# Performance work log

Hardware: AMD Instinct MI355X
Metric: run time of the kernel (lower is better)

The kernel has to match this reference:

```python
import jax, jax.numpy as jnp
import numpy as np

NUM_GRAPHS = 64


def gcn_conv(x, edge_index, W, b):
    # PyG GCNConv: x' = D^-1/2 (A+I) D^-1/2 (x W) + b, self-loops added.
    n = x.shape[0]
    h = x @ W  # [N, out]
    loop = jnp.arange(n)
    src = jnp.concatenate([edge_index[0], loop])
    dst = jnp.concatenate([edge_index[1], loop])
    deg = jax.ops.segment_sum(jnp.ones_like(dst, dtype=h.dtype), dst, num_segments=n)
    dinv = jnp.where(deg > 0, jax.lax.rsqrt(deg), 0.0)
    norm = dinv[src] * dinv[dst]  # [E+N]
    msgs = h[src] * norm[:, None]  # gather + scale
    out = jax.ops.segment_sum(msgs, dst, num_segments=n)  # scatter-add
    return out + b


def lstm_step(x, W_ih, W_hh, b_ih, b_hh):
    # single time step, zero initial state; PyTorch gate order i,f,g,o
    H = W_hh.shape[1]
    gates = x @ W_ih.T + b_ih + b_hh  # h0 = 0 so W_hh term vanishes
    i, f, g, o = jnp.split(gates, 4, axis=-1)
    i, f, o = jax.nn.sigmoid(i), jax.nn.sigmoid(f), jax.nn.sigmoid(o)
    c = i * jnp.tanh(g)  # f * c0 = 0
    return o * jnp.tanh(c)


def setup_inputs() -> dict:
    key = jax.random.key(0)
    ks = jax.random.split(key, 16)
    N, E, F, G, H, C = 50000, 600000, 128, 128, 256, 1
    s = lambda *sh: 1.0 / np.sqrt(sh[-1])
    return {
        "x": jax.random.normal(ks[0], (N, F), jnp.float32),
        "edge_index": jax.random.randint(ks[1], (2, E), 0, N),
        "batch": jnp.sort(jax.random.randint(ks[2], (N,), 0, NUM_GRAPHS)),
        "W1": jax.random.normal(ks[3], (F, G), jnp.float32) * s(F, G),
        "b1": jnp.zeros((G,), jnp.float32),
        "W2": jax.random.normal(ks[4], (G, G), jnp.float32) * s(G, G),
        "b2": jnp.zeros((G,), jnp.float32),
        "W_ih": jax.random.normal(ks[5], (4 * H, G), jnp.float32) * s(4 * H, G),
        "W_hh": jax.random.normal(ks[6], (4 * H, H), jnp.float32) * s(4 * H, H),
        "b_ih": jnp.zeros((4 * H,), jnp.float32),
        "b_hh": jnp.zeros((4 * H,), jnp.float32),
        "Wm": jax.random.normal(ks[7], (C, H), jnp.float32) * s(C, H),
        "bm": jnp.zeros((C,), jnp.float32),
        "Wv": jax.random.normal(ks[8], (C, H), jnp.float32) * s(C, H),
        "bv": jnp.zeros((C,), jnp.float32),
    }


def reference(x, edge_index, batch, W1, b1, W2, b2, W_ih, W_hh, b_ih, b_hh, Wm, bm, Wv, bv):
    h = jax.nn.relu(gcn_conv(x, edge_index, W1, b1))
    h = jax.nn.relu(gcn_conv(h, edge_index, W2, b2))
    # global mean pool over graphs
    sums = jax.ops.segment_sum(h, batch, num_segments=NUM_GRAPHS)
    cnts = jax.ops.segment_sum(jnp.ones_like(batch, dtype=h.dtype), batch, num_segments=NUM_GRAPHS)
    pooled = sums / jnp.maximum(cnts, 1.0)[:, None]  # [G_graphs, gcn_hidden]
    hT = lstm_step(pooled, W_ih, W_hh, b_ih, b_hh)  # [G_graphs, lstm_hidden]
    mean = hT @ Wm.T + bm
    log_var = jax.nn.softplus(hT @ Wv.T + bv)
    return (mean, log_var)
```

## Files before the change

kernel.cpp:

```cpp
#include <hip/hip_runtime.h>
#include <hip/hip_bf16.h>
#include <math.h>


#define POOL_SUB 32

#if __has_builtin(__builtin_amdgcn_cvt_pk_f32_fp8) && __has_builtin(__builtin_amdgcn_cvt_pk_fp8_f32)
#define USE_FP8 1
#else
#define USE_FP8 0
#endif

typedef __attribute__((ext_vector_type(8))) short bf16x8;
typedef __attribute__((ext_vector_type(4))) float f32x4;
typedef __attribute__((ext_vector_type(2))) float f32x2;

static __device__ __forceinline__ unsigned short f2bf(float f) {
    union { float f; unsigned int u; } v; v.f = f;
    unsigned int u = v.u;
    unsigned int r = u + 0x7FFFu + ((u >> 16) & 1u);
    return (unsigned short)(r >> 16);
}
static __device__ __forceinline__ unsigned int pack2bf(float lo, float hi) {
    return (unsigned int)f2bf(lo) | ((unsigned int)f2bf(hi) << 16);
}
static __device__ __forceinline__ float bflo(unsigned int v) {
    union { unsigned int u; float f; } w; w.u = v << 16; return w.f;
}
static __device__ __forceinline__ float bfhi(unsigned int v) {
    union { unsigned int u; float f; } w; w.u = v & 0xFFFF0000u; return w.f;
}
static __device__ __forceinline__ bf16x8 f8_to_bf(float4 f0, float4 f1) {
    union { unsigned int u[4]; bf16x8 v; } r;
    r.u[0] = pack2bf(f0.x, f0.y);
    r.u[1] = pack2bf(f0.z, f0.w);
    r.u[2] = pack2bf(f1.x, f1.y);
    r.u[3] = pack2bf(f1.z, f1.w);
    return r.v;
}
#if USE_FP8
static __device__ __forceinline__ unsigned char f2fp8(float f) {
    return (unsigned char)(__builtin_amdgcn_cvt_pk_fp8_f32(f, f, 0, false) & 0xFF);
}
#endif

__global__ __launch_bounds__(256) void prep_kernel(int* __restrict__ zp, int zwords,
                                                   const float* __restrict__ W1,
                                                   const float* __restrict__ W2,
                                                   unsigned short* __restrict__ Wt1,
                                                   unsigned short* __restrict__ Wt2, int zb) {
    int b = blockIdx.x;
    int t = threadIdx.x;
    if (b < zb) {
        int i = b * 256 + t;
        if (i < zwords) zp[i] = 0;
    } else {
        int col = b - zb;
        if (t < 128) Wt1[col * 128 + t] = f2bf(W1[(size_t)t * 128 + col]);
        else { int k = t - 128; Wt2[col * 128 + k] = f2bf(W2[(size_t)k * 128 + col]); }
    }
}

__global__ void count_deg_kernel(const int* __restrict__ dst, int E, int* __restrict__ deg) {
    int e = blockIdx.x * blockDim.x + threadIdx.x;
    if (e < E) atomicAdd(&deg[dst[e]], 1);
}

__global__ void scan_pass1(const int* __restrict__ deg, int n,
                           int* __restrict__ rowptr, int* __restrict__ bsums) {
    __shared__ int s[256];
    int tid = threadIdx.x;
    int base = blockIdx.x * 1024;
    int v[4];
    int mysum = 0;
#pragma unroll
    for (int j = 0; j < 4; ++j) {
        int idx = base + tid * 4 + j;
        v[j] = (idx < n) ? deg[idx] : 0;
        mysum += v[j];
    }
    s[tid] = mysum;
    __syncthreads();
    for (int off = 1; off < 256; off <<= 1) {
        int t = (tid >= off) ? s[tid - off] : 0;
        __syncthreads();
        s[tid] += t;
        __syncthreads();
    }
    int excl = s[tid] - mysum;
#pragma unroll
    for (int j = 0; j < 4; ++j) {
        int idx = base + tid * 4 + j;
        if (idx < n) rowptr[idx] = excl;
        excl += v[j];
    }
    if (tid == 255) bsums[blockIdx.x] = s[255];
}

__global__ void scan_pass23(int* __restrict__ rowptr, const int* __restrict__ bsums,
                            const int* __restrict__ deg, float* __restrict__ dinv,
                            int n, int nb) {
    __shared__ int sm[64];
    __shared__ int pref[65];
    int tid = threadIdx.x;
    if (tid < 64) sm[tid] = (tid < nb) ? bsums[tid] : 0;
    __syncthreads();
    if (tid == 0) {
        int s = 0;
#pragma unroll 8
        for (int i = 0; i < 64; ++i) { pref[i] = s; s += sm[i]; }
        pref[64] = s;
    }
    __syncthreads();
    int add = pref[blockIdx.x];
    int base = blockIdx.x * 1024;
#pragma unroll
    for (int j = 0; j < 4; ++j) {
        int idx = base + tid * 4 + j;
        if (idx < n) {
            rowptr[idx] += add;
            dinv[idx] = rsqrtf((float)deg[idx] + 1.0f);
        }
    }
    if (blockIdx.x == 0 && tid == 0) rowptr[n] = pref[64];
}

__global__ void fill_csr_kernel(const int* __restrict__ src, const int* __restrict__ dst, int E,
                                const int* __restrict__ rowptr, int* __restrict__ cursor,
                                int* __restrict__ csr) {
    int e = blockIdx.x * blockDim.x + threadIdx.x;
    if (e < E) {
        int d = dst[e];
        int pos = rowptr[d] + atomicAdd(&cursor[d], 1);
        csr[pos] = src[e];
    }
}


#if USE_FP8
#define G_STORE(outp, row, col, val) ((unsigned char*)(outp))[(size_t)(row) * 128 + (col)] = f2fp8(val)
#else
#define G_STORE(outp, row, col, val) ((unsigned short*)(outp))[(size_t)(row) * 128 + (col)] = f2bf(val)
#endif

__global__ __launch_bounds__(256) void gemm_mfma_f32a_kernel(const float* __restrict__ A,
                                                             const unsigned short* __restrict__ Wt,
                                                             const float* __restrict__ dinv,
                                                             void* __restrict__ out,
                                                             int n) {
    int tid = threadIdx.x;
    int l = tid & 63;
    int wid = tid >> 6;
    int rowbase = blockIdx.x * 64 + wid * 16;
    int lc = l & 15;
    int kq = l >> 4;

    int arow = rowbase + lc; if (arow > n - 1) arow = n - 1;
    const float* Ap = A + (size_t)arow * 128 + kq * 8;
    const unsigned short* Wp = Wt + (size_t)lc * 128 + kq * 8;

    f32x4 acc[8];
#pragma unroll
    for (int c = 0; c < 8; ++c) acc[c] = (f32x4){0.f, 0.f, 0.f, 0.f};

#pragma unroll
    for (int ks = 0; ks < 4; ++ks) {
        float4 f0 = *(const float4*)(Ap + ks * 32);
        float4 f1 = *(const float4*)(Ap + ks * 32 + 4);
        bf16x8 a = f8_to_bf(f0, f1);
#pragma unroll
        for (int c = 0; c < 8; ++c) {
            bf16x8 b = *(const bf16x8*)(Wp + c * 2048 + ks * 32);
            acc[c] = __builtin_amdgcn_mfma_f32_16x16x32_bf16(a, b, acc[c], 0, 0, 0);
        }
    }

    int r0 = kq * 4;
    float s[4];
    int orow[4];
#pragma unroll
    for (int r = 0; r < 4; ++r) {
        orow[r] = rowbase + r0 + r;
        s[r] = (orow[r] < n) ? dinv[orow[r]] : 0.f;
    }
#pragma unroll
    for (int c = 0; c < 8; ++c) {
#pragma unroll
        for (int r = 0; r < 4; ++r) {
            if (orow[r] < n) G_STORE(out, orow[r], c * 16 + lc, acc[c][r] * s[r]);
        }
    }
}

__global__ __launch_bounds__(256) void gemm_mfma_kernel(const unsigned short* __restrict__ A,
                                                        const unsigned short* __restrict__ Wt,
                                                        const float* __restrict__ dinv,
                                                        void* __restrict__ out,
                                                        int n) {
    int tid = threadIdx.x;
    int l = tid & 63;
    int wid = tid >> 6;
    int rowbase = blockIdx.x * 64 + wid * 16;
    int lc = l & 15;
    int kq = l >> 4;

    int arow = rowbase + lc; if (arow > n - 1) arow = n - 1;
    const unsigned short* Ap = A + (size_t)arow * 128 + kq * 8;
    const unsigned short* Wp = Wt + (size_t)lc * 128 + kq * 8;

    f32x4 acc[8];
#pragma unroll
    for (int c = 0; c < 8; ++c) acc[c] = (f32x4){0.f, 0.f, 0.f, 0.f};

#pragma unroll
    for (int ks = 0; ks < 4; ++ks) {
        bf16x8 a = *(const bf16x8*)(Ap + ks * 32);
#pragma unroll
        for (int c = 0; c < 8; ++c) {
            bf16x8 b = *(const bf16x8*)(Wp + c * 2048 + ks * 32);
            acc[c] = __builtin_amdgcn_mfma_f32_16x16x32_bf16(a, b, acc[c], 0, 0, 0);
        }
    }

    int r0 = kq * 4;
    float s[4];
    int orow[4];
#pragma unroll
    for (int r = 0; r < 4; ++r) {
        orow[r] = rowbase + r0 + r;
        s[r] = (orow[r] < n) ? dinv[orow[r]] : 0.f;
    }
#pragma unroll
    for (int c = 0; c < 8; ++c) {
#pragma unroll
        for (int r = 0; r < 4; ++r) {
            if (orow[r] < n) G_STORE(out, orow[r], c * 16 + lc, acc[c][r] * s[r]);
        }
    }
}

#if USE_FP8
__global__ __launch_bounds__(256) void aggregate_kernel(const void* __restrict__ gv,
                                                        const int* __restrict__ rowptr,
                                                        const int* __restrict__ csr,
                                                        const float* __restrict__ dinv,
                                                        const float* __restrict__ bias,
                                                        unsigned int* __restrict__ out, int n) {
    const uint2* __restrict__ g2 = (const uint2*)gv;
    int lane = threadIdx.x & 63;
    int node = (blockIdx.x * blockDim.x + threadIdx.x) >> 6;
    if (node >= n) return;
    int li = lane & 15, quad = lane >> 4;
    int beg = rowptr[node], end = rowptr[node + 1];
    float a0 = 0.f, a1 = 0.f, a2 = 0.f, a3 = 0.f;
    float a4 = 0.f, a5 = 0.f, a6 = 0.f, a7 = 0.f;
    int e = beg;
    for (; e + 4 <= end; e += 4) {
        uint2 v = g2[(size_t)csr[e + quad] * 16 + li];
        f32x2 p0 = __builtin_amdgcn_cvt_pk_f32_fp8(v.x, false);
        f32x2 p1 = __builtin_amdgcn_cvt_pk_f32_fp8(v.x, true);
        f32x2 p2 = __builtin_amdgcn_cvt_pk_f32_fp8(v.y, false);
        f32x2 p3 = __builtin_amdgcn_cvt_pk_f32_fp8(v.y, true);
        a0 += p0.x; a1 += p0.y; a2 += p1.x; a3 += p1.y;
        a4 += p2.x; a5 += p2.y; a6 += p3.x; a7 += p3.y;
    }
    if (e + quad < end) {
        uint2 v = g2[(size_t)csr[e + quad] * 16 + li];
        f32x2 p0 = __builtin_amdgcn_cvt_pk_f32_fp8(v.x, false);
        f32x2 p1 = __builtin_amdgcn_cvt_pk_f32_fp8(v.x, true);
        f32x2 p2 = __builtin_amdgcn_cvt_pk_f32_fp8(v.y, false);
        f32x2 p3 = __builtin_amdgcn_cvt_pk_f32_fp8(v.y, true);
        a0 += p0.x; a1 += p0.y; a2 += p1.x; a3 += p1.y;
        a4 += p2.x; a5 += p2.y; a6 += p3.x; a7 += p3.y;
    }
    a0 += __shfl_xor(a0, 16, 64); a0 += __shfl_xor(a0, 32, 64);
    a1 += __shfl_xor(a1, 16, 64); a1 += __shfl_xor(a1, 32, 64);
    a2 += __shfl_xor(a2, 16, 64); a2 += __shfl_xor(a2, 32, 64);
    a3 += __shfl_xor(a3, 16, 64); a3 += __shfl_xor(a3, 32, 64);
    a4 += __shfl_xor(a4, 16, 64); a4 += __shfl_xor(a4, 32, 64);
    a5 += __shfl_xor(a5, 16, 64); a5 += __shfl_xor(a5, 32, 64);
    a6 += __shfl_xor(a6, 16, 64); a6 += __shfl_xor(a6, 32, 64);
    a7 += __shfl_xor(a7, 16, 64); a7 += __shfl_xor(a7, 32, 64);
    if (quad == 0) {
        uint2 sv = g2[(size_t)node * 16 + li];
        f32x2 s0 = __builtin_amdgcn_cvt_pk_f32_fp8(sv.x, false);
        f32x2 s1 = __builtin_amdgcn_cvt_pk_f32_fp8(sv.x, true);
        f32x2 s2 = __builtin_amdgcn_cvt_pk_f32_fp8(sv.y, false);
        f32x2 s3 = __builtin_amdgcn_cvt_pk_f32_fp8(sv.y, true);
        float dv = dinv[node];
        float4 bl = ((const float4*)bias)[li * 2];
        float4 bh = ((const float4*)bias)[li * 2 + 1];
        float r0 = fmaxf(dv * (a0 + s0.x) + bl.x, 0.f);
        float r1 = fmaxf(dv * (a1 + s0.y) + bl.y, 0.f);
        float r2 = fmaxf(dv * (a2 + s1.x) + bl.z, 0.f);
        float r3 = fmaxf(dv * (a3 + s1.y) + bl.w, 0.f);
        float r4 = fmaxf(dv * (a4 + s2.x) + bh.x, 0.f);
        float r5 = fmaxf(dv * (a5 + s2.y) + bh.y, 0.f);
        float r6 = fmaxf(dv * (a6 + s3.x) + bh.z, 0.f);
        float r7 = fmaxf(dv * (a7 + s3.y) + bh.w, 0.f);
        uint4 o;
        o.x = pack2bf(r0, r1); o.y = pack2bf(r2, r3);
        o.z = pack2bf(r4, r5); o.w = pack2bf(r6, r7);
        ((uint4*)out)[(size_t)node * 16 + li] = o;
    }
}
#else
__global__ __launch_bounds__(256) void aggregate_kernel(const void* __restrict__ gv,
                                                        const int* __restrict__ rowptr,
                                                        const int* __restrict__ csr,
                                                        const float* __restrict__ dinv,
                                                        const float* __restrict__ bias,
                                                        unsigned int* __restrict__ out, int n) {
    const uint2* __restrict__ g2 = (const uint2*)gv;
    int lane = threadIdx.x & 63;
    int node = (blockIdx.x * blockDim.x + threadIdx.x) >> 6;
    if (node >= n) return;
    int li = lane & 31, pair = lane >> 5;
    int beg = rowptr[node], end = rowptr[node + 1];
    float a0 = 0.f, a1 = 0.f, a2 = 0.f, a3 = 0.f;
    int e = beg;
    for (; e + 2 <= end; e += 2) {
        uint2 v = g2[(size_t)csr[e + pair] * 32 + li];
        a0 += bflo(v.x); a1 += bfhi(v.x);
        a2 += bflo(v.y); a3 += bfhi(v.y);
    }
    if (e + pair < end) {
        uint2 v = g2[(size_t)csr[e + pair] * 32 + li];
        a0 += bflo(v.x); a1 += bfhi(v.x);
        a2 += bflo(v.y); a3 += bfhi(v.y);
    }
    a0 += __shfl_xor(a0, 32, 64);
    a1 += __shfl_xor(a1, 32, 64);
    a2 += __shfl_xor(a2, 32, 64);
    a3 += __shfl_xor(a3, 32, 64);
    if (pair == 0) {
        uint2 sv = g2[(size_t)node * 32 + li];
        float dv = dinv[node];
        float4 b = ((const float4*)bias)[li];
        float r0 = fmaxf(dv * (a0 + bflo(sv.x)) + b.x, 0.f);
        float r1 = fmaxf(dv * (a1 + bfhi(sv.x)) + b.y, 0.f);
        float r2 = fmaxf(dv * (a2 + bflo(sv.y)) + b.z, 0.f);
        float r3 = fmaxf(dv * (a3 + bfhi(sv.y)) + b.w, 0.f);
        ((uint2*)out)[(size_t)node * 32 + li] = make_uint2(pack2bf(r0, r1), pack2bf(r2, r3));
    }
}
#endif

__global__ __launch_bounds__(64) void pool_partial_kernel(const unsigned int* __restrict__ h,
                                                          const int* __restrict__ batch, int n,
                                                          float* __restrict__ partial) {
    int g = blockIdx.x / POOL_SUB;
    int sub = blockIdx.x % POOL_SUB;
    int t = threadIdx.x;
    int lo = 0, hi = n;
    while (lo < hi) { int mid = (lo + hi) >> 1; if (batch[mid] < g) lo = mid + 1; else hi = mid; }
    int start = lo;
    hi = n;
    while (lo < hi) { int mid = (lo + hi) >> 1; if (batch[mid] < g + 1) lo = mid + 1; else hi = mid; }
    int end = lo;
    int len = end - start;
    int b0 = start + (int)((long long)len * sub / POOL_SUB);
    int b1 = start + (int)((long long)len * (sub + 1) / POOL_SUB);
    float ax = 0.f, ay = 0.f;
    int i = b0;
    for (; i + 4 <= b1; i += 4) {
        unsigned int v0 = h[(size_t)(i + 0) * 64 + t];
        unsigned int v1 = h[(size_t)(i + 1) * 64 + t];
        unsigned int v2 = h[(size_t)(i + 2) * 64 + t];
        unsigned int v3 = h[(size_t)(i + 3) * 64 + t];
        ax += bflo(v0) + bflo(v1) + bflo(v2) + bflo(v3);
        ay += bfhi(v0) + bfhi(v1) + bfhi(v2) + bfhi(v3);
    }
    for (; i < b1; ++i) {
        unsigned int v0 = h[(size_t)i * 64 + t];
        ax += bflo(v0);
        ay += bfhi(v0);
    }
    partial[(size_t)blockIdx.x * 128 + 2 * t]     = ax;
    partial[(size_t)blockIdx.x * 128 + 2 * t + 1] = ay;
}

__global__ __launch_bounds__(256) void pool_lstm_kernel(const float* __restrict__ partial,
                                                        const int* __restrict__ batch, int n,
                                                        const float* __restrict__ W_ih,
                                                        const float* __restrict__ b_ih,
                                                        const float* __restrict__ b_hh,
                                                        const float* __restrict__ Wm,
                                                        const float* __restrict__ bm,
                                                        const float* __restrict__ Wv,
                                                        const float* __restrict__ bv,
                                                        float* __restrict__ out) {
    __shared__ __align__(16) float p[128];
    __shared__ float redm[256];
    __shared__ float redv[256];
    int gph = blockIdx.x;
    int tid = threadIdx.x;
    if (tid < 128) {
        int lo = 0, hi = n;
        while (lo < hi) { int mid = (lo + hi) >> 1; if (batch[mid] < gph) lo = mid + 1; else hi = mid; }
        int start = lo;
        hi = n;
        while (lo < hi) { int mid = (lo + hi) >> 1; if (batch[mid] < gph + 1) lo = mid + 1; else hi = mid; }
        int end = lo;
        float acc = 0.f;
#pragma unroll
        for (int s = 0; s < POOL_SUB; ++s)
            acc += partial[(size_t)(gph * POOL_SUB + s) * 128 + tid];
        p[tid] = acc / fmaxf((float)(end - start), 1.0f);
    }
    __syncthreads();
    float gi = b_ih[tid] + b_hh[tid];
    float gg = b_ih[512 + tid] + b_hh[512 + tid];
    float go = b_ih[768 + tid] + b_hh[768 + tid];
    const float4* wi = (const float4*)(W_ih + (size_t)tid * 128);
    const float4* wg = (const float4*)(W_ih + (size_t)(512 + tid) * 128);
    const float4* wo = (const float4*)(W_ih + (size_t)(768 + tid) * 128);
    const float4* p4 = (const float4*)p;
#pragma unroll 8
    for (int k = 0; k < 32; ++k) {
        float4 xv = p4[k];
        float4 a = wi[k], bq = wg[k], cq = wo[k];
        gi += xv.x * a.x + xv.y * a.y + xv.z * a.z + xv.w * a.w;
        gg += xv.x * bq.x + xv.y * bq.y + xv.z * bq.z + xv.w * bq.w;
        go += xv.x * cq.x + xv.y * cq.y + xv.z * cq.z + xv.w * cq.w;
    }
    float iv = 1.f / (1.f + expf(-gi));
    float cv = iv * tanhf(gg);
    float ov = 1.f / (1.f + expf(-go));
    float hT = ov * tanhf(cv);
    redm[tid] = hT * Wm[tid];
    redv[tid] = hT * Wv[tid];
    __syncthreads();
    for (int s = 128; s > 0; s >>= 1) {
        if (tid < s) { redm[tid] += redm[tid + s]; redv[tid] += redv[tid + s]; }
        __syncthreads();
    }
    if (tid == 0) {
        out[gph] = redm[0] + bm[0];
        float xv = redv[0] + bv[0];
        out[64 + gph] = fmaxf(xv, 0.f) + log1pf(expf(-fabsf(xv)));
    }
}

extern "C" void kernel_launch(void* const* d_in, const int* in_sizes, int n_in,
                              void* d_out, int out_size, void* d_ws, size_t ws_size,
                              hipStream_t stream) {
    const float* x     = (const float*)d_in[0];
    const int*   edge  = (const int*)d_in[1];
    const int*   batch = (const int*)d_in[2];
    const float* W1    = (const float*)d_in[3];
    const float* b1    = (const float*)d_in[4];
    const float* W2    = (const float*)d_in[5];
    const float* b2    = (const float*)d_in[6];
    const float* W_ih  = (const float*)d_in[7];
    const float* b_ih  = (const float*)d_in[9];
    const float* b_hh  = (const float*)d_in[10];
    const float* Wm    = (const float*)d_in[11];
    const float* bm    = (const float*)d_in[12];
    const float* Wv    = (const float*)d_in[13];
    const float* bv    = (const float*)d_in[14];
    float* out = (float*)d_out;

    const int N = in_sizes[0] / 128;
    const int E = in_sizes[1] / 2;
    const int* srcIdx = edge;
    const int* dstIdx = edge + E;

    char* ws = (char*)d_ws;
    size_t off = 0;
    const size_t gB = (size_t)N * 64 * sizeof(unsigned int);
    void* gbuf = (void*)(ws + off); off += gB;
    unsigned int* hbuf = (unsigned int*)(ws + off); off += gB;
    int* deg    = (int*)(ws + off);   off += (size_t)N * sizeof(int);
    int* cursor = (int*)(ws + off);   off += (size_t)N * sizeof(int);
    int* rowptr = (int*)(ws + off);   off += (size_t)(N + 1) * sizeof(int);
    off = (off + 255) & ~(size_t)255;
    int* bsums  = (int*)(ws + off);   off += 512;
    int* csr    = (int*)(ws + off);   off += (size_t)E * sizeof(int);
    off = (off + 255) & ~(size_t)255;
    float* dinv = (float*)(ws + off); off += (size_t)N * sizeof(float);
    off = (off + 255) & ~(size_t)255;
    unsigned short* Wt1 = (unsigned short*)(ws + off); off += 128 * 128 * sizeof(unsigned short);
    unsigned short* Wt2 = (unsigned short*)(ws + off); off += 128 * 128 * sizeof(unsigned short);
    off = (off + 255) & ~(size_t)255;
    float* partial = (float*)(ws + off); off += (size_t)64 * POOL_SUB * 128 * sizeof(float);

    int zwords = 2 * N;
    int zb = (zwords + 255) / 256;
    prep_kernel<<<zb + 128, 256, 0, stream>>>(deg, zwords, W1, W2, Wt1, Wt2, zb);

    int eb = (E + 255) / 256;
    count_deg_kernel<<<eb, 256, 0, stream>>>(dstIdx, E, deg);

    int nb = (N + 1023) / 1024;
    scan_pass1<<<nb, 256, 0, stream>>>(deg, N, rowptr, bsums);
    scan_pass23<<<nb, 256, 0, stream>>>(rowptr, bsums, deg, dinv, N, nb);
    fill_csr_kernel<<<eb, 256, 0, stream>>>(srcIdx, dstIdx, E, rowptr, cursor, csr);

    int gb = (N + 63) / 64;
    int ab = (N + 3) / 4;

    gemm_mfma_f32a_kernel<<<gb, 256, 0, stream>>>(x, Wt1, dinv, gbuf, N);
    aggregate_kernel<<<ab, 256, 0, stream>>>(gbuf, rowptr, csr, dinv, b1, hbuf, N);
    gemm_mfma_kernel<<<gb, 256, 0, stream>>>((const unsigned short*)hbuf, Wt2, dinv, gbuf, N);
    aggregate_kernel<<<ab, 256, 0, stream>>>(gbuf, rowptr, csr, dinv, b2, hbuf, N);

    pool_partial_kernel<<<64 * POOL_SUB, 64, 0, stream>>>(hbuf, batch, N, partial);
    pool_lstm_kernel<<<64, 256, 0, stream>>>(partial, batch, N, W_ih, b_ih, b_hh, Wm, bm, Wv, bv, out);
}
```

Baseline: 209.0 us.

## Fuse whole GCN pipeline into one cooperative persistent megakernel with grid syncs

Replaces the sequence of eleven kernel launches (zeroing, degree count, scan, CSR fill, two GEMMs, two aggregations, pooling, LSTM head) with a single cooperative persistent kernel. Each phase runs as a grid-stride loop over tiles and phases are separated by grid-wide barriers. The original multi-kernel path is kept as a fallback when cooperative launch is unavailable. This targets per-launch overhead and inter-kernel gaps. In exchange it adds grid.sync costs, limits resident blocks and occupancy per phase, and fixes the grid size for phases with very different parallelism.

Result: slower. 792.5 us (+279.2%).

```diff
diff --git a/kernel.cpp b/kernel.cpp
--- a/kernel.cpp
+++ b/kernel.cpp
@@ -1,6 +1,9 @@
 #include <hip/hip_runtime.h>
+#include <hip/hip_cooperative_groups.h>
 #include <hip/hip_bf16.h>
 #include <math.h>
+
+namespace cg = cooperative_groups;
 
 
 #define POOL_SUB 32
@@ -44,219 +47,111 @@
 }
 #endif
 
-__global__ __launch_bounds__(256) void prep_kernel(int* __restrict__ zp, int zwords,
-                                                   const float* __restrict__ W1,
-                                                   const float* __restrict__ W2,
-                                                   unsigned short* __restrict__ Wt1,
-                                                   unsigned short* __restrict__ Wt2, int zb) {
-    int b = blockIdx.x;
-    int t = threadIdx.x;
-    if (b < zb) {
-        int i = b * 256 + t;
-        if (i < zwords) zp[i] = 0;
-    } else {
-        int col = b - zb;
-        if (t < 128) Wt1[col * 128 + t] = f2bf(W1[(size_t)t * 128 + col]);
-        else { int k = t - 128; Wt2[col * 128 + k] = f2bf(W2[(size_t)k * 128 + col]); }
-    }
-}
-
-__global__ void count_deg_kernel(const int* __restrict__ dst, int E, int* __restrict__ deg) {
-    int e = blockIdx.x * blockDim.x + threadIdx.x;
-    if (e < E) atomicAdd(&deg[dst[e]], 1);
-}
-
-__global__ void scan_pass1(const int* __restrict__ deg, int n,
-                           int* __restrict__ rowptr, int* __restrict__ bsums) {
-    __shared__ int s[256];
+struct MegaArgs {
+    const float* x;
+    const int* src; const int* dst; const int* batch;
+    const float* W1; const float* b1; const float* W2; const float* b2;
+    const float* W_ih; const float* b_ih; const float* b_hh;
+    const float* Wm; const float* bm; const float* Wv; const float* bv;
+    float* out;
+    void* gbuf;
+    unsigned int* hbuf;
+    int* deg; int* cursor; int* rowptr; int* bsums; int* csr;
+    float* dinv;
+    unsigned short* Wt1; unsigned short* Wt2;
+    float* partial;
+    int N, E, nchunks, gb, ab;
+};
+
+#if USE_FP8
+#define STORE_G(p, row, col, val) ((unsigned char*)(p))[(size_t)(row) * 128 + (col)] = f2fp8(val)
+#else
+#define STORE_G(p, row, col, val) ((unsigned short*)(p))[(size_t)(row) * 128 + (col)] = f2bf(val)
+#endif
+
+
+__device__ __forceinline__ void gemm_tile_f32a(int t, const MegaArgs& a) {
     int tid = threadIdx.x;
-    int base = blockIdx.x * 1024;
-    int v[4];
-    int mysum = 0;
-#pragma unroll
-    for (int j = 0; j < 4; ++j) {
-        int idx = base + tid * 4 + j;
-        v[j] = (idx < n) ? deg[idx] : 0;
-        mysum += v[j];
-    }
-    s[tid] = mysum;
-    __syncthreads();
-    for (int off = 1; off < 256; off <<= 1) {
-        int t = (tid >= off) ? s[tid - off] : 0;
-        __syncthreads();
-        s[tid] += t;
-        __syncthreads();
-    }
-    int excl = s[tid] - mysum;
-#pragma unroll
-    for (int j = 0; j < 4; ++j) {
-        int idx = base + tid * 4 + j;
-        if (idx < n) rowptr[idx] = excl;
-        excl += v[j];
-    }
-    if (tid == 255) bsums[blockIdx.x] = s[255];
-}
-
-__global__ void scan_pass23(int* __restrict__ rowptr, const int* __restrict__ bsums,
-                            const int* __restrict__ deg, float* __restrict__ dinv,
-                            int n, int nb) {
-    __shared__ int sm[64];
-    __shared__ int pref[65];
-    int tid = threadIdx.x;
-    if (tid < 64) sm[tid] = (tid < nb) ? bsums[tid] : 0;
-    __syncthreads();
-    if (tid == 0) {
-        int s = 0;
-#pragma unroll 8
-        for (int i = 0; i < 64; ++i) { pref[i] = s; s += sm[i]; }
-        pref[64] = s;
-    }
-    __syncthreads();
-    int add = pref[blockIdx.x];
-    int base = blockIdx.x * 1024;
-#pragma unroll
-    for (int j = 0; j < 4; ++j) {
-        int idx = base + tid * 4 + j;
-        if (idx < n) {
-            rowptr[idx] += add;
-            dinv[idx] = rsqrtf((float)deg[idx] + 1.0f);
-        }
-    }
-    if (blockIdx.x == 0 && tid == 0) rowptr[n] = pref[64];
-}
-
-__global__ void fill_csr_kernel(const int* __restrict__ src, const int* __restrict__ dst, int E,
-                                const int* __restrict__ rowptr, int* __restrict__ cursor,
-                                int* __restrict__ csr) {
-    int e = blockIdx.x * blockDim.x + threadIdx.x;
-    if (e < E) {
-        int d = dst[e];
-        int pos = rowptr[d] + atomicAdd(&cursor[d], 1);
-        csr[pos] = src[e];
-    }
-}
-
-
-#if USE_FP8
-#define G_STORE(outp, row, col, val) ((unsigned char*)(outp))[(size_t)(row) * 128 + (col)] = f2fp8(val)
-#else
-#define G_STORE(outp, row, col, val) ((unsigned short*)(outp))[(size_t)(row) * 128 + (col)] = f2bf(val)
-#endif
-
-__global__ __launch_bounds__(256) void gemm_mfma_f32a_kernel(const float* __restrict__ A,
-                                                             const unsigned short* __restrict__ Wt,
-                                                             const float* __restrict__ dinv,
-                                                             void* __restrict__ out,
-                                                             int n) {
-    int tid = threadIdx.x;
-    int l = tid & 63;
-    int wid = tid >> 6;
-    int rowbase = blockIdx.x * 64 + wid * 16;
-    int lc = l & 15;
-    int kq = l >> 4;
-
+    int l = tid & 63, wid = tid >> 6;
+    int rowbase = t * 64 + wid * 16;
+    int lc = l & 15, kq = l >> 4;
+    int n = a.N;
     int arow = rowbase + lc; if (arow > n - 1) arow = n - 1;
-    const float* Ap = A + (size_t)arow * 128 + kq * 8;
-    const unsigned short* Wp = Wt + (size_t)lc * 128 + kq * 8;
-
+    const float* Ap = a.x + (size_t)arow * 128 + kq * 8;
+    const unsigned short* Wp = a.Wt1 + (size_t)lc * 128 + kq * 8;
     f32x4 acc[8];
 #pragma unroll
     for (int c = 0; c < 8; ++c) acc[c] = (f32x4){0.f, 0.f, 0.f, 0.f};
-
 #pragma unroll
     for (int ks = 0; ks < 4; ++ks) {
         float4 f0 = *(const float4*)(Ap + ks * 32);
         float4 f1 = *(const float4*)(Ap + ks * 32 + 4);
-        bf16x8 a = f8_to_bf(f0, f1);
+        bf16x8 av = f8_to_bf(f0, f1);
 #pragma unroll
         for (int c = 0; c < 8; ++c) {
-            bf16x8 b = *(const bf16x8*)(Wp + c * 2048 + ks * 32);
-            acc[c] = __builtin_amdgcn_mfma_f32_16x16x32_bf16(a, b, acc[c], 0, 0, 0);
-        }
-    }
-
+            bf16x8 bv = *(const bf16x8*)(Wp + c * 2048 + ks * 32);
+            acc[c] = __builtin_amdgcn_mfma_f32_16x16x32_bf16(av, bv, acc[c], 0, 0, 0);
+        }
+    }
     int r0 = kq * 4;
-    float s[4];
-    int orow[4];
 #pragma unroll
     for (int r = 0; r < 4; ++r) {
-        orow[r] = rowbase + r0 + r;
-        s[r] = (orow[r] < n) ? dinv[orow[r]] : 0.f;
-    }
-#pragma unroll
-    for (int c = 0; c < 8; ++c) {
-#pragma unroll
-        for (int r = 0; r < 4; ++r) {
-            if (orow[r] < n) G_STORE(out, orow[r], c * 16 + lc, acc[c][r] * s[r]);
-        }
-    }
-}
-
-__global__ __launch_bounds__(256) void gemm_mfma_kernel(const unsigned short* __restrict__ A,
-                                                        const unsigned short* __restrict__ Wt,
-                                                        const float* __restrict__ dinv,
-                                                        void* __restrict__ out,
-                                                        int n) {
+        int orow = rowbase + r0 + r;
+        if (orow < n) {
+            float s = a.dinv[orow];
+#pragma unroll
+            for (int c = 0; c < 8; ++c) STORE_G(a.gbuf, orow, c * 16 + lc, acc[c][r] * s);
+        }
+    }
+}
+
+__device__ __forceinline__ void gemm_tile_h(int t, const MegaArgs& a) {
     int tid = threadIdx.x;
-    int l = tid & 63;
-    int wid = tid >> 6;
-    int rowbase = blockIdx.x * 64 + wid * 16;
-    int lc = l & 15;
-    int kq = l >> 4;
-
+    int l = tid & 63, wid = tid >> 6;
+    int rowbase = t * 64 + wid * 16;
+    int lc = l & 15, kq = l >> 4;
+    int n = a.N;
     int arow = rowbase + lc; if (arow > n - 1) arow = n - 1;
-    const unsigned short* Ap = A + (size_t)arow * 128 + kq * 8;
-    const unsigned short* Wp = Wt + (size_t)lc * 128 + kq * 8;
-
+    const unsigned short* Ap = (const unsigned short*)a.hbuf + (size_t)arow * 128 + kq * 8;
+    const unsigned short* Wp = a.Wt2 + (size_t)lc * 128 + kq * 8;
     f32x4 acc[8];
 #pragma unroll
     for (int c = 0; c < 8; ++c) acc[c] = (f32x4){0.f, 0.f, 0.f, 0.f};
-
 #pragma unroll
     for (int ks = 0; ks < 4; ++ks) {
-        bf16x8 a = *(const bf16x8*)(Ap + ks * 32);
+        bf16x8 av = *(const bf16x8*)(Ap + ks * 32);
 #pragma unroll
         for (int c = 0; c < 8; ++c) {
-            bf16x8 b = *(const bf16x8*)(Wp + c * 2048 + ks * 32);
-            acc[c] = __builtin_amdgcn_mfma_f32_16x16x32_bf16(a, b, acc[c], 0, 0, 0);
-        }
-    }
-
+            bf16x8 bv = *(const bf16x8*)(Wp + c * 2048 + ks * 32);
+            acc[c] = __builtin_amdgcn_mfma_f32_16x16x32_bf16(av, bv, acc[c], 0, 0, 0);
+        }
+    }
     int r0 = kq * 4;
-    float s[4];
-    int orow[4];
 #pragma unroll
     for (int r = 0; r < 4; ++r) {
-        orow[r] = rowbase + r0 + r;
-        s[r] = (orow[r] < n) ? dinv[orow[r]] : 0.f;
-    }
-#pragma unroll
-    for (int c = 0; c < 8; ++c) {
-#pragma unroll
-        for (int r = 0; r < 4; ++r) {
-            if (orow[r] < n) G_STORE(out, orow[r], c * 16 + lc, acc[c][r] * s[r]);
-        }
-    }
-}
-
+        int orow = rowbase + r0 + r;
+        if (orow < n) {
+            float s = a.dinv[orow];
+#pragma unroll
+            for (int c = 0; c < 8; ++c) STORE_G(a.gbuf, orow, c * 16 + lc, acc[c][r] * s);
+        }
+    }
+}
+
+__device__ __forceinline__ void agg_group(int grp, const float* bias, const MegaArgs& a) {
+    int lane = threadIdx.x & 63;
+    int wid = threadIdx.x >> 6;
+    int node = grp * 4 + wid;
+    if (node >= a.N) return;
+    int beg = a.rowptr[node], end = a.rowptr[node + 1];
 #if USE_FP8
-__global__ __launch_bounds__(256) void aggregate_kernel(const void* __restrict__ gv,
-                                                        const int* __restrict__ rowptr,
-                                                        const int* __restrict__ csr,
-                                                        const float* __restrict__ dinv,
-                                                        const float* __restrict__ bias,
-                                                        unsigned int* __restrict__ out, int n) {
-    const uint2* __restrict__ g2 = (const uint2*)gv;
-    int lane = threadIdx.x & 63;
-    int node = (blockIdx.x * blockDim.x + threadIdx.x) >> 6;
-    if (node >= n) return;
+    const uint2* g2 = (const uint2*)a.gbuf;
     int li = lane & 15, quad = lane >> 4;
-    int beg = rowptr[node], end = rowptr[node + 1];
     float a0 = 0.f, a1 = 0.f, a2 = 0.f, a3 = 0.f;
     float a4 = 0.f, a5 = 0.f, a6 = 0.f, a7 = 0.f;
     int e = beg;
     for (; e + 4 <= end; e += 4) {
-        uint2 v = g2[(size_t)csr[e + quad] * 16 + li];
+        uint2 v = g2[(size_t)a.csr[e + quad] * 16 + li];
         f32x2 p0 = __builtin_amdgcn_cvt_pk_f32_fp8(v.x, false);
         f32x2 p1 = __builtin_amdgcn_cvt_pk_f32_fp8(v.x, true);
         f32x2 p2 = __builtin_amdgcn_cvt_pk_f32_fp8(v.y, false);
@@ -265,7 +160,7 @@
         a4 += p2.x; a5 += p2.y; a6 += p3.x; a7 += p3.y;
     }
     if (e + quad < end) {
-        uint2 v = g2[(size_t)csr[e + quad] * 16 + li];
+        uint2 v = g2[(size_t)a.csr[e + quad] * 16 + li];
         f32x2 p0 = __builtin_amdgcn_cvt_pk_f32_fp8(v.x, false);
         f32x2 p1 = __builtin_amdgcn_cvt_pk_f32_fp8(v.x, true);
         f32x2 p2 = __builtin_amdgcn_cvt_pk_f32_fp8(v.y, false);
@@ -287,7 +182,7 @@
         f32x2 s1 = __builtin_amdgcn_cvt_pk_f32_fp8(sv.x, true);
         f32x2 s2 = __builtin_amdgcn_cvt_pk_f32_fp8(sv.y, false);
         f32x2 s3 = __builtin_amdgcn_cvt_pk_f32_fp8(sv.y, true);
-        float dv = dinv[node];
+        float dv = a.dinv[node];
         float4 bl = ((const float4*)bias)[li * 2];
         float4 bh = ((const float4*)bias)[li * 2 + 1];
         float r0 = fmaxf(dv * (a0 + s0.x) + bl.x, 0.f);
@@ -301,31 +196,20 @@
         uint4 o;
         o.x = pack2bf(r0, r1); o.y = pack2bf(r2, r3);
         o.z = pack2bf(r4, r5); o.w = pack2bf(r6, r7);
-        ((uint4*)out)[(size_t)node * 16 + li] = o;
-    }
-}
+        ((uint4*)a.hbuf)[(size_t)node * 16 + li] = o;
+    }
 #else
-__global__ __launch_bounds__(256) void aggregate_kernel(const void* __restrict__ gv,
-                                                        const int* __restrict__ rowptr,
-                                                        const int* __restrict__ csr,
-                                                        const float* __restrict__ dinv,
-                                                        const float* __restrict__ bias,
-                                                        unsigned int* __restrict__ out, int n) {
-    const uint2* __restrict__ g2 = (const uint2*)gv;
-    int lane = threadIdx.x & 63;
-    int node = (blockIdx.x * blockDim.x + threadIdx.x) >> 6;
-    if (node >= n) return;
+    const uint2* g2 = (const uint2*)a.gbuf;
     int li = lane & 31, pair = lane >> 5;
-    int beg = rowptr[node], end = rowptr[node + 1];
     float a0 = 0.f, a1 = 0.f, a2 = 0.f, a3 = 0.f;
     int e = beg;
     for (; e + 2 <= end; e += 2) {
-        uint2 v = g2[(size_t)csr[e + pair] * 32 + li];
+        uint2 v = g2[(size_t)a.csr[e + pair] * 32 + li];
         a0 += bflo(v.x); a1 += bfhi(v.x);
         a2 += bflo(v.y); a3 += bfhi(v.y);
     }
     if (e + pair < end) {
-        uint2 v = g2[(size_t)csr[e + pair] * 32 + li];
+        uint2 v = g2[(size_t)a.csr[e + pair] * 32 + li];
         a0 += bflo(v.x); a1 += bfhi(v.x);
         a2 += bflo(v.y); a3 += bfhi(v.y);
     }
@@ -335,28 +219,26 @@
     a3 += __shfl_xor(a3, 32, 64);
     if (pair == 0) {
         uint2 sv = g2[(size_t)node * 32 + li];
-        float dv = dinv[node];
+        float dv = a.dinv[node];
         float4 b = ((const float4*)bias)[li];
         float r0 = fmaxf(dv * (a0 + bflo(sv.x)) + b.x, 0.f);
         float r1 = fmaxf(dv * (a1 + bfhi(sv.x)) + b.y, 0.f);
         float r2 = fmaxf(dv * (a2 + bflo(sv.y)) + b.z, 0.f);
         float r3 = fmaxf(dv * (a3 + bfhi(sv.y)) + b.w, 0.f);
-        ((uint2*)out)[(size_t)node * 32 + li] = make_uint2(pack2bf(r0, r1), pack2bf(r2, r3));
-    }
-}
+        ((uint2*)a.hbuf)[(size_t)node * 32 + li] = make_uint2(pack2bf(r0, r1), pack2bf(r2, r3));
+    }
 #endif
-
-__global__ __launch_bounds__(64) void pool_partial_kernel(const unsigned int* __restrict__ h,
-                                                          const int* __restrict__ batch, int n,
-                                                          float* __restrict__ partial) {
-    int g = blockIdx.x / POOL_SUB;
-    int sub = blockIdx.x % POOL_SUB;
-    int t = threadIdx.x;
+}
+
+__device__ __forceinline__ void pool_partial_unit(int unit, int t, const MegaArgs& a) {
+    int g = unit / POOL_SUB;
+    int sub = unit % POOL_SUB;
+    int n = a.N;
     int lo = 0, hi = n;
-    while (lo < hi) { int mid = (lo + hi) >> 1; if (batch[mid] < g) lo = mid + 1; else hi = mid; }
+    while (lo < hi) { int mid = (lo + hi) >> 1; if (a.batch[mid] < g) lo = mid + 1; else hi = mid; }
     int start = lo;
     hi = n;
-    while (lo < hi) { int mid = (lo + hi) >> 1; if (batch[mid] < g + 1) lo = mid + 1; else hi = mid; }
+    while (lo < hi) { int mid = (lo + hi) >> 1; if (a.batch[mid] < g + 1) lo = mid + 1; else hi = mid; }
     int end = lo;
     int len = end - start;
     int b0 = start + (int)((long long)len * sub / POOL_SUB);
@@ -364,63 +246,53 @@
     float ax = 0.f, ay = 0.f;
     int i = b0;
     for (; i + 4 <= b1; i += 4) {
-        unsigned int v0 = h[(size_t)(i + 0) * 64 + t];
-        unsigned int v1 = h[(size_t)(i + 1) * 64 + t];
-        unsigned int v2 = h[(size_t)(i + 2) * 64 + t];
-        unsigned int v3 = h[(size_t)(i + 3) * 64 + t];
+        unsigned int v0 = a.hbuf[(size_t)(i + 0) * 64 + t];
+        unsigned int v1 = a.hbuf[(size_t)(i + 1) * 64 + t];
+        unsigned int v2 = a.hbuf[(size_t)(i + 2) * 64 + t];
+        unsigned int v3 = a.hbuf[(size_t)(i + 3) * 64 + t];
         ax += bflo(v0) + bflo(v1) + bflo(v2) + bflo(v3);
         ay += bfhi(v0) + bfhi(v1) + bfhi(v2) + bfhi(v3);
     }
     for (; i < b1; ++i) {
-        unsigned int v0 = h[(size_t)i * 64 + t];
+        unsigned int v0 = a.hbuf[(size_t)i * 64 + t];
         ax += bflo(v0);
         ay += bfhi(v0);
     }
-    partial[(size_t)blockIdx.x * 128 + 2 * t]     = ax;
-    partial[(size_t)blockIdx.x * 128 + 2 * t + 1] = ay;
-}
-
-__global__ __launch_bounds__(256) void pool_lstm_kernel(const float* __restrict__ partial,
-                                                        const int* __restrict__ batch, int n,
-                                                        const float* __restrict__ W_ih,
-                                                        const float* __restrict__ b_ih,
-                                                        const float* __restrict__ b_hh,
-                                                        const float* __restrict__ Wm,
-                                                        const float* __restrict__ bm,
-                                                        const float* __restrict__ Wv,
-                                                        const float* __restrict__ bv,
-                                                        float* __restrict__ out) {
-    __shared__ __align__(16) float p[128];
-    __shared__ float redm[256];
-    __shared__ float redv[256];
-    int gph = blockIdx.x;
+    a.partial[(size_t)unit * 128 + 2 * t]     = ax;
+    a.partial[(size_t)unit * 128 + 2 * t + 1] = ay;
+}
+
+__device__ __forceinline__ void pool_lstm_graph(int g, float* shraw, const MegaArgs& a) {
+    float* p = shraw;
+    float* redm = p + 128;
+    float* redv = redm + 256;
     int tid = threadIdx.x;
     if (tid < 128) {
-        int lo = 0, hi = n;
-        while (lo < hi) { int mid = (lo + hi) >> 1; if (batch[mid] < gph) lo = mid + 1; else hi = mid; }
+        int lo = 0, hi = a.N;
+        while (lo < hi) { int mid = (lo + hi) >> 1; if (a.batch[mid] < g) lo = mid + 1; else hi = mid; }
         int start = lo;
-        hi = n;
-        while (lo < hi) { int mid = (lo + hi) >> 1; if (batch[mid] < gph + 1) lo = mid + 1; else hi = mid; }
+        hi = a.N;
+        while (lo < hi) { int mid = (lo + hi) >> 1; if (a.batch[mid] < g + 1) lo = mid + 1; else hi = mid; }
         int end = lo;
         float acc = 0.f;
 #pragma unroll
         for (int s = 0; s < POOL_SUB; ++s)
-            acc += partial[(size_t)(gph * POOL_SUB + s) * 128 + tid];
+            acc += a.partial[(size_t)(g * POOL_SUB + s) * 128 + tid];
         p[tid] = acc / fmaxf((float)(end - start), 1.0f);
     }
     __syncthreads();
-    float gi = b_ih[tid] + b_hh[tid];
-    float gg = b_ih[512 + tid] + b_hh[512 + tid];
-    float go = b_ih[768 + tid] + b_hh[768 + tid];
-    const float4* wi = (const float4*)(W_ih + (size_t)tid * 128);
-    const float4* wg = (const float4*)(W_ih + (size_t)(512 + tid) * 128);
-    const float4* wo = (const float4*)(W_ih + (size_t)(768 + tid) * 128);
+    float gi = a.b_ih[tid] + a.b_hh[tid];
+    float gg = a.b_ih[512 + tid] + a.b_hh[512 + tid];
+    float go = a.b_ih[768 + tid] + a.b_hh[768 + tid];
+    const float4* wi = (const float4*)(a.W_ih + (size_t)tid * 128);
+    const float4* wg = (const float4*)(a.W_ih + (size_t)(512 + tid) * 128);
+    const float4* wo = (const float4*)(a.W_ih + (size_t)(768 + tid) * 128);
     const float4* p4 = (const float4*)p;
 #pragma unroll 8
     for (int k = 0; k < 32; ++k) {
         float4 xv = p4[k];
-        float4 a = wi[k], bq = wg[k], cq = wo[k];
-        gi += xv.x * a.x + xv.y * a.y + xv.z * a.z + xv.w * a.w;
+        float4 aq = wi[k], bq = wg[k], cq = wo[k];
+        gi += xv.x * aq.x + xv.y * aq.y + xv.z * aq.z + xv.w * aq.w;
         gg += xv.x * bq.x + xv.y * bq.y + xv.z * bq.z + xv.w * bq.w;
         go += xv.x * cq.x + xv.y * cq.y + xv.z * cq.z + xv.w * cq.w;
     }
@@ -428,83 +300,290 @@
     float cv = iv * tanhf(gg);
     float ov = 1.f / (1.f + expf(-go));
     float hT = ov * tanhf(cv);
-    redm[tid] = hT * Wm[tid];
-    redv[tid] = hT * Wv[tid];
+    redm[tid] = hT * a.Wm[tid];
+    redv[tid] = hT * a.Wv[tid];
     __syncthreads();
     for (int s = 128; s > 0; s >>= 1) {
         if (tid < s) { redm[tid] += redm[tid + s]; redv[tid] += redv[tid + s]; }
         __syncthreads();
     }
     if (tid == 0) {
-        out[gph] = redm[0] + bm[0];
-        float xv = redv[0] + bv[0];
-        out[64 + gph] = fmaxf(xv, 0.f) + log1pf(expf(-fabsf(xv)));
-    }
+        a.out[g] = redm[0] + a.bm[0];
+        float xv = redv[0] + a.bv[0];
+        a.out[64 + g] = fmaxf(xv, 0.f) + log1pf(expf(-fabsf(xv)));
+    }
+    __syncthreads();
+}
+
+
+__global__ __launch_bounds__(256, 4) void mega_kernel(MegaArgs a) {
+    cg::grid_group grid = cg::this_grid();
+    __shared__ __align__(16) float shraw[656];
+    int tid = threadIdx.x;
+    int bid = blockIdx.x;
+    int G = gridDim.x;
+    int gstride = G * 256;
+    int gtid = bid * 256 + tid;
+
+    int zwords = 2 * a.N;
+    for (int i = gtid; i < zwords; i += gstride) a.deg[i] = 0;
+    for (int i = gtid; i < 128 * 128; i += gstride) {
+        int col = i >> 7, k = i & 127;
+        a.Wt1[col * 128 + k] = f2bf(a.W1[(size_t)k * 128 + col]);
+        a.Wt2[col * 128 + k] = f2bf(a.W2[(size_t)k * 128 + col]);
+    }
+    grid.sync();
+
+    for (int e = gtid; e < a.E; e += gstride) atomicAdd(&a.deg[a.dst[e]], 1);
+    grid.sync();
+
+    {
+        int* s = (int*)shraw;
+        for (int c = bid; c < a.nchunks; c += G) {
+            int base = c * 1024;
+            int v[4];
+            int mysum = 0;
+#pragma unroll
+            for (int j = 0; j < 4; ++j) {
+                int idx = base + tid * 4 + j;
+                v[j] = (idx < a.N) ? a.deg[idx] : 0;
+                mysum += v[j];
+            }
+            s[tid] = mysum;
+            __syncthreads();
+            for (int off = 1; off < 256; off <<= 1) {
+                int t2 = (tid >= off) ? s[tid - off] : 0;
+                __syncthreads();
+                s[tid] += t2;
+                __syncthreads();
+            }
+            int excl = s[tid] - mysum;
+#pragma unroll
+            for (int j = 0; j < 4; ++j) {
+                int idx = base + tid * 4 + j;
+                if (idx < a.N) a.rowptr[idx] = excl;
+                excl += v[j];
+            }
+            if (tid == 255) a.bsums[c] = s[255];
+            __syncthreads();
+        }
+    }
+    grid.sync();
+
+    {
+        int* sm = (int*)shraw;
+        int* pref = sm + 64;
+        if (tid < 64) sm[tid] = (tid < a.nchunks) ? a.bsums[tid] : 0;
+        __syncthreads();
+        if (tid == 0) {
+            int s2 = 0;
+            for (int i = 0; i < 64; ++i) { pref[i] = s2; s2 += sm[i]; }
+            pref[64] = s2;
+        }
+        __syncthreads();
+        for (int c = bid; c < a.nchunks; c += G) {
+            int add = pref[c];
+            int base = c * 1024;
+#pragma unroll
+            for (int j = 0; j < 4; ++j) {
+                int idx = base + tid * 4 + j;
+                if (idx < a.N) {
+                    a.rowptr[idx] += add;
+                    a.dinv[idx] = rsqrtf((float)a.deg[idx] + 1.0f);
+                }
+            }
+        }
+        if (bid == 0 && tid == 0) a.rowptr[a.N] = pref[64];
+    }
+    grid.sync();
+
+    for (int e = gtid; e < a.E; e += gstride) {
+        int d = a.dst[e];
+        int pos = a.rowptr[d] + atomicAdd(&a.cursor[d], 1);
+        a.csr[pos] = a.src[e];
+    }
+    for (int t = bid; t < a.gb; t += G) gemm_tile_f32a(t, a);
+    grid.sync();
+
+    for (int grp = bid; grp < a.ab; grp += G) agg_group(grp, a.b1, a);
+    grid.sync();
+
+    for (int t = bid; t < a.gb; t += G) gemm_tile_h(t, a);
+    grid.sync();
+
+    for (int grp = bid; grp < a.ab; grp += G) agg_group(grp, a.b2, a);
+    grid.sync();
+
+    for (int grp = bid; grp < (64 * POOL_SUB) / 4; grp += G)
+        pool_partial_unit(grp * 4 + (tid >> 6), tid & 63, a);
+    grid.sync();
+
+    for (int g = bid; g < 64; g += G) pool_lstm_graph(g, shraw, a);
+}
+
+
+__global__ __launch_bounds__(256) void k_p0(MegaArgs a) {
+    int gtid = blockIdx.x * 256 + threadIdx.x, gstride = gridDim.x * 256;
+    for (int i = gtid; i < 2 * a.N; i += gstride) a.deg[i] = 0;
+    for (int i = gtid; i < 128 * 128; i += gstride) {
+        int col = i >> 7, k = i & 127;
+        a.Wt1[col * 128 + k] = f2bf(a.W1[(size_t)k * 128 + col]);
+        a.Wt2[col * 128 + k] = f2bf(a.W2[(size_t)k * 128 + col]);
+    }
+}
+__global__ void k_count(MegaArgs a) {
+    int e = blockIdx.x * 256 + threadIdx.x;
+    if (e < a.E) atomicAdd(&a.deg[a.dst[e]], 1);
+}
+__global__ void k_scan1(MegaArgs a) {
+    __shared__ int s[256];
+    int tid = threadIdx.x;
+    int base = blockIdx.x * 1024;
+    int v[4];
+    int mysum = 0;
+#pragma unroll
+    for (int j = 0; j < 4; ++j) {
+        int idx = base + tid * 4 + j;
+        v[j] = (idx < a.N) ? a.deg[idx] : 0;
+        mysum += v[j];
+    }
+    s[tid] = mysum;
+    __syncthreads();
+    for (int off = 1; off < 256; off <<= 1) {
+        int t = (tid >= off) ? s[tid - off] : 0;
+        __syncthreads();
+        s[tid] += t;
+        __syncthreads();
+    }
+    int excl = s[tid] - mysum;
+#pragma unroll
+    for (int j = 0; j < 4; ++j) {
+        int idx = base + tid * 4 + j;
+        if (idx < a.N) a.rowptr[idx] = excl;
+        excl += v[j];
+    }
+    if (tid == 255) a.bsums[blockIdx.x] = s[255];
+}
+__global__ void k_scan23(MegaArgs a) {
+    __shared__ int sm[64];
+    __shared__ int pref[65];
+    int tid = threadIdx.x;
+    if (tid < 64) sm[tid] = (tid < a.nchunks) ? a.bsums[tid] : 0;
+    __syncthreads();
+    if (tid == 0) {
+        int s = 0;
+        for (int i = 0; i < 64; ++i) { pref[i] = s; s += sm[i]; }
+        pref[64] = s;
+    }
+    __syncthreads();
+    int add = pref[blockIdx.x];
+    int base = blockIdx.x * 1024;
+#pragma unroll
+    for (int j = 0; j < 4; ++j) {
+        int idx = base + tid * 4 + j;
+        if (idx < a.N) {
+            a.rowptr[idx] += add;
+            a.dinv[idx] = rsqrtf((float)a.deg[idx] + 1.0f);
+        }
+    }
+    if (blockIdx.x == 0 && tid == 0) a.rowptr[a.N] = pref[64];
+}
+__global__ void k_csr(MegaArgs a) {
+    int e = blockIdx.x * 256 + threadIdx.x;
+    if (e < a.E) {
+        int d = a.dst[e];
+        int pos = a.rowptr[d] + atomicAdd(&a.cursor[d], 1);
+        a.csr[pos] = a.src[e];
+    }
+}
+__global__ __launch_bounds__(256) void k_gemm1(MegaArgs a) { gemm_tile_f32a(blockIdx.x, a); }
+__global__ __launch_bounds__(256) void k_gemm2(MegaArgs a) { gemm_tile_h(blockIdx.x, a); }
+__global__ __launch_bounds__(256) void k_agg1(MegaArgs a) { agg_group(blockIdx.x, a.b1, a); }
+__global__ __launch_bounds__(256) void k_agg2(MegaArgs a) { agg_group(blockIdx.x, a.b2, a); }
+__global__ __launch_bounds__(64) void k_poolp(MegaArgs a) { pool_partial_unit(blockIdx.x, threadIdx.x, a); }
+__global__ __launch_bounds__(256) void k_plstm(MegaArgs a) {
+    __shared__ __align__(16) float shraw[656];
+    pool_lstm_graph(blockIdx.x, shraw, a);
 }
 
 extern "C" void kernel_launch(void* const* d_in, const int* in_sizes, int n_in,
                               void* d_out, int out_size, void* d_ws, size_t ws_size,
                               hipStream_t stream) {
-    const float* x     = (const float*)d_in[0];
-    const int*   edge  = (const int*)d_in[1];
-    const int*   batch = (const int*)d_in[2];
-    const float* W1    = (const float*)d_in[3];
-    const float* b1    = (const float*)d_in[4];
-    const float* W2    = (const float*)d_in[5];
-    const float* b2    = (const float*)d_in[6];
-    const float* W_ih  = (const float*)d_in[7];
-    const float* b_ih  = (const float*)d_in[9];
-    const float* b_hh  = (const float*)d_in[10];
-    const float* Wm    = (const float*)d_in[11];
-    const float* bm    = (const float*)d_in[12];
-    const float* Wv    = (const float*)d_in[13];
-    const float* bv    = (const float*)d_in[14];
-    float* out = (float*)d_out;
+    MegaArgs A;
+    A.x     = (const float*)d_in[0];
+    const int* edge = (const int*)d_in[1];
+    A.batch = (const int*)d_in[2];
+    A.W1    = (const float*)d_in[3];
+    A.b1    = (const float*)d_in[4];
+    A.W2    = (const float*)d_in[5];
+    A.b2    = (const float*)d_in[6];
+    A.W_ih  = (const float*)d_in[7];
+    A.b_ih  = (const float*)d_in[9];
+    A.b_hh  = (const float*)d_in[10];
+    A.Wm    = (const float*)d_in[11];
+    A.bm    = (const float*)d_in[12];
+    A.Wv    = (const float*)d_in[13];
+    A.bv    = (const float*)d_in[14];
+    A.out   = (float*)d_out;
 
     const int N = in_sizes[0] / 128;
     const int E = in_sizes[1] / 2;
-    const int* srcIdx = edge;
-    const int* dstIdx = edge + E;
+    A.src = edge;
+    A.dst = edge + E;
+    A.N = N;
+    A.E = E;
+    A.nchunks = (N + 1023) / 1024;
+    A.gb = (N + 63) / 64;
+    A.ab = (N + 3) / 4;
 
     char* ws = (char*)d_ws;
     size_t off = 0;
     const size_t gB = (size_t)N * 64 * sizeof(unsigned int);
-    void* gbuf = (void*)(ws + off); off += gB;
-    unsigned int* hbuf = (unsigned int*)(ws + off); off += gB;
-    int* deg    = (int*)(ws + off);   off += (size_t)N * sizeof(int);
-    int* cursor = (int*)(ws + off);   off += (size_t)N * sizeof(int);
-    int* rowptr = (int*)(ws + off);   off += (size_t)(N + 1) * sizeof(int);
+    A.gbuf = (void*)(ws + off); off += gB;
+    A.hbuf = (unsigned int*)(ws + off); off += gB;
+    A.deg    = (int*)(ws + off); off += (size_t)N * sizeof(int);
+    A.cursor = (int*)(ws + off); off += (size_t)N * sizeof(int);
+    A.rowptr = (int*)(ws + off); off += (size_t)(N + 1) * sizeof(int);
     off = (off + 255) & ~(size_t)255;
-    int* bsums  = (int*)(ws + off);   off += 512;
-    int* csr    = (int*)(ws + off);   off += (size_t)E * sizeof(int);
+    A.bsums = (int*)(ws + off); off += 512;
+    A.csr   = (int*)(ws + off); off += (size_t)E * sizeof(int);
     off = (off + 255) & ~(size_t)255;
-    float* dinv = (float*)(ws + off); off += (size_t)N * sizeof(float);
+    A.dinv = (float*)(ws + off); off += (size_t)N * sizeof(float);
     off = (off + 255) & ~(size_t)255;
-    unsigned short* Wt1 = (unsigned short*)(ws + off); off += 128 * 128 * sizeof(unsigned short);
-    unsigned short* Wt2 = (unsigned short*)(ws + off); off += 128 * 128 * sizeof(unsigned short);
+    A.Wt1 = (unsigned short*)(ws + off); off += 128 * 128 * sizeof(unsigned short);
+    A.Wt2 = (unsigned short*)(ws + off); off += 128 * 128 * sizeof(unsigned short);
     off = (off + 255) & ~(size_t)255;
-    float* partial = (float*)(ws + off); off += (size_t)64 * POOL_SUB * 128 * sizeof(float);
-
-    int zwords = 2 * N;
-    int zb = (zwords + 255) / 256;
-    prep_kernel<<<zb + 128, 256, 0, stream>>>(deg, zwords, W1, W2, Wt1, Wt2, zb);
+    A.partial = (float*)(ws + off); off += (size_t)64 * POOL_SUB * 128 * sizeof(float);
+
+    hipError_t le = hipErrorUnknown;
+    int dev = 0;
+    if (hipGetDevice(&dev) == hipSuccess) {
+        int coop = 0;
+        hipDeviceGetAttribute(&coop, hipDeviceAttributeCooperativeLaunch, dev);
+        int numCU = 0;
+        hipDeviceGetAttribute(&numCU, hipDeviceAttributeMultiprocessorCount, dev);
+        int maxB = 0;
+        hipError_t oe = hipOccupancyMaxActiveBlocksPerMultiprocessor(&maxB, mega_kernel, 256, 0);
+        if (coop && numCU > 0 && oe == hipSuccess && maxB > 0) {
+            if (maxB > 8) maxB = 8;
+            int G = numCU * maxB;
+            void* kargs[] = { (void*)&A };
+            le = hipLaunchCooperativeKernel((const void*)mega_kernel, dim3(G), dim3(256),
+                                            kargs, 0, stream);
+        }
+    }
+    if (le == hipSuccess) return;
 
     int eb = (E + 255) / 256;
-    count_deg_kernel<<<eb, 256, 0, stream>>>(dstIdx, E, deg);
-
-    int nb = (N + 1023) / 1024;
-    scan_pass1<<<nb, 256, 0, stream>>>(deg, N, rowptr, bsums);
-    scan_pass23<<<nb, 256, 0, stream>>>(rowptr, bsums, deg, dinv, N, nb);
-    fill_csr_kernel<<<eb, 256, 0, stream>>>(srcIdx, dstIdx, E, rowptr, cursor, csr);
-
-    int gb = (N + 63) / 64;
-    int ab = (N + 3) / 4;
-
-    gemm_mfma_f32a_kernel<<<gb, 256, 0, stream>>>(x, Wt1, dinv, gbuf, N);
-    aggregate_kernel<<<ab, 256, 0, stream>>>(gbuf, rowptr, csr, dinv, b1, hbuf, N);
-    gemm_mfma_kernel<<<gb, 256, 0, stream>>>((const unsigned short*)hbuf, Wt2, dinv, gbuf, N);
-    aggregate_kernel<<<ab, 256, 0, stream>>>(gbuf, rowptr, csr, dinv, b2, hbuf, N);
-
-    pool_partial_kernel<<<64 * POOL_SUB, 64, 0, stream>>>(hbuf, batch, N, partial);
-    pool_lstm_kernel<<<64, 256, 0, stream>>>(partial, batch, N, W_ih, b_ih, b_hh, Wm, bm, Wv, bv, out);
-}
+    k_p0<<<400, 256, 0, stream>>>(A);
+    k_count<<<eb, 256, 0, stream>>>(A);
+    k_scan1<<<A.nchunks, 256, 0, stream>>>(A);
+    k_scan23<<<A.nchunks, 256, 0, stream>>>(A);
+    k_csr<<<eb, 256, 0, stream>>>(A);
+    k_gemm1<<<A.gb, 256, 0, stream>>>(A);
+    k_agg1<<<A.ab, 256, 0, stream>>>(A);
+    k_gemm2<<<A.gb, 256, 0, stream>>>(A);
+    k_agg2<<<A.ab, 256, 0, stream>>>(A);
+    k_poolp<<<64 * POOL_SUB, 64, 0, stream>>>(A);
+    k_plstm<<<64, 256, 0, stream>>>(A);
+}
```
